# Performance work log

Hardware: AMD Instinct MI355X
Metric: run time of the kernel (lower is better)

Reference implementation:

```python
import jax, jax.numpy as jnp
import numpy as np

N_NODES = 100000
N_EDGES = 1600000
F_IN = 32
F_OUT = 32


def setup_inputs() -> dict:
    key = jax.random.key(0)
    k_x, k_r, k_c, k_v, k_w, k_b = jax.random.split(key, 6)
    x = jax.random.normal(k_x, (N_NODES, F_IN), dtype=jnp.float32)
    edge_rows = jnp.sort(jax.random.randint(k_r, (N_EDGES,), 0, N_NODES, dtype=jnp.int32))
    edge_cols = jax.random.randint(k_c, (N_EDGES,), 0, N_NODES, dtype=jnp.int32)
    edge_vals = jax.random.uniform(k_v, (N_EDGES,), dtype=jnp.float32)
    # nn.Linear params: weight [out, in], bias [out]
    bound = 1.0 / np.sqrt(F_IN)
    W = jax.random.uniform(k_w, (F_OUT, F_IN), minval=-bound, maxval=bound, dtype=jnp.float32)
    b = jax.random.uniform(k_b, (F_OUT,), minval=-bound, maxval=bound, dtype=jnp.float32)
    return {"x": x, "edge_rows": edge_rows, "edge_cols": edge_cols,
            "edge_vals": edge_vals, "W": W, "b": b}


def reference(x, edge_rows, edge_cols, edge_vals, W, b):
    # adj @ x  (COO spmm): gather source features, scale by edge weight,
    # scatter-add into destination rows.
    msgs = x[edge_cols] * edge_vals[:, None]                 # [E, F_in]
    agg = jax.ops.segment_sum(msgs, edge_rows,
                              num_segments=x.shape[0],
                              indices_are_sorted=True)       # [N, F_in]
    # linear + relu: agg @ W.T + b
    return jax.nn.relu(agg @ W.T + b)                        # [N, F_out]
```

## Files before the change

### kernel.cpp

```cpp
#include <hip/hip_runtime.h>

#define F 32

typedef __attribute__((ext_vector_type(8))) unsigned short us8;
typedef __attribute__((ext_vector_type(4))) float f4;

static __device__ __forceinline__ unsigned short f2bf(float f) {
    unsigned int u = __float_as_uint(f);
    u += 0x7FFF + ((u >> 16) & 1);
    return (unsigned short)(u >> 16);
}
static __device__ __forceinline__ float bf2f(unsigned short s) {
    return __uint_as_float(((unsigned int)s) << 16);
}

__global__ __launch_bounds__(256) void prologue_kernel(
    const float* __restrict__ x, const float* __restrict__ W,
    const int* __restrict__ rows,
    unsigned short* __restrict__ y, int* __restrict__ ptr,
    int N, int E, int nxw) {
    int b = blockIdx.x;
    int t = threadIdx.x;
    if (b < nxw) {
        __shared__ float Wt[F * F];
        __shared__ float xs[64 * F];
        #pragma unroll
        for (int k = 0; k < 4; ++k) {
            int i = t + k * 256;
            Wt[(i & 31) * F + (i >> 5)] = W[i];
        }
        int n0 = b * 64;
        const f4* __restrict__ x4 = (const f4*)(x + (size_t)n0 * F);
        f4* __restrict__ xs4 = (f4*)xs;
        int limit4 = (N * F - n0 * F) >> 2;
        #pragma unroll
        for (int k = 0; k < 2; ++k) {
            int i = t + k * 256;
            f4 z = {0.f, 0.f, 0.f, 0.f};
            xs4[i] = (i < limit4) ? x4[i] : z;
        }
        __syncthreads();
        int fo = t & 31;
        int j0 = (t >> 5) * 8;
        #pragma unroll
        for (int j = 0; j < 8; ++j) {
            int nl = j0 + j;
            float acc = 0.0f;
            #pragma unroll
            for (int fi = 0; fi < F; ++fi)
                acc = fmaf(xs[nl * F + fi], Wt[fi * F + fo], acc);
            int n = n0 + nl;
            if (n < N) y[(size_t)n * F + fo] = f2bf(acc);
        }
    } else {
        int e = (b - nxw) * 256 + t;
        if (e > E) return;
        int prev = (e == 0) ? -1 : rows[e - 1];
        int cur  = (e == E) ? N  : rows[e];
        for (int r = prev + 1; r <= cur; ++r) ptr[r] = e;
    }
}

__global__ __launch_bounds__(256) void gnn_kernel(
    const unsigned short* __restrict__ y,
    const int*   __restrict__ cols,
    const float* __restrict__ vals,
    const int*   __restrict__ row_ptr,
    const float* __restrict__ bias,
    float*       __restrict__ out, int N) {
    int t = threadIdx.x;
    int lane = t & 63;
    int g = lane >> 2;
    int l = lane & 3;
    int n = (blockIdx.x * 4 + (t >> 6)) * 16 + g;
    int start = 0, end = 0;
    if (n < N) { start = row_ptr[n]; end = row_ptr[n + 1]; }

    const us8* __restrict__ y8 = (const us8*)y;

    float a0[8], a1[8];
    #pragma unroll
    for (int i = 0; i < 8; ++i) { a0[i] = 0.f; a1[i] = 0.f; }

    for (int e = start; e < end; e += 8) {
        int ec[8];
        #pragma unroll
        for (int k = 0; k < 8; ++k) {
            int ek = e + k;
            ec[k] = (ek < end) ? ek : (end - 1);
        }
        int c[8];
        #pragma unroll
        for (int k = 0; k < 8; ++k) c[k] = cols[ec[k]];
        float v[8];
        #pragma unroll
        for (int k = 0; k < 8; ++k) {
            float vv = vals[ec[k]];
            v[k] = (e + k < end) ? vv : 0.0f;
        }
        us8 r[8];
        #pragma unroll
        for (int k = 0; k < 8; ++k) r[k] = y8[(size_t)c[k] * 4 + l];
        #pragma unroll
        for (int k = 0; k < 8; ++k) {
            float* a = (k & 1) ? a1 : a0;
            #pragma unroll
            for (int i = 0; i < 8; ++i)
                a[i] = fmaf(bf2f(r[k][i]), v[k], a[i]);
        }
    }

    if (n < N) {
        const float* __restrict__ bp = bias + l * 8;
        f4 o0, o1;
        o0.x = fmaxf(a0[0] + a1[0] + bp[0], 0.f);
        o0.y = fmaxf(a0[1] + a1[1] + bp[1], 0.f);
        o0.z = fmaxf(a0[2] + a1[2] + bp[2], 0.f);
        o0.w = fmaxf(a0[3] + a1[3] + bp[3], 0.f);
        o1.x = fmaxf(a0[4] + a1[4] + bp[4], 0.f);
        o1.y = fmaxf(a0[5] + a1[5] + bp[5], 0.f);
        o1.z = fmaxf(a0[6] + a1[6] + bp[6], 0.f);
        o1.w = fmaxf(a0[7] + a1[7] + bp[7], 0.f);
        f4* op = (f4*)(out + (size_t)n * F + l * 8);
        __builtin_nontemporal_store(o0, op);
        __builtin_nontemporal_store(o1, op + 1);
    }
}

__global__ __launch_bounds__(256) void gnn_fp32_kernel(
    const float* __restrict__ x,
    const int*   __restrict__ rows,
    const int*   __restrict__ cols,
    const float* __restrict__ vals,
    const float* __restrict__ W,
    const float* __restrict__ bias,
    float*       __restrict__ out,
    int N, int E) {
    __shared__ float Wt[F * F];
    __shared__ float bS[F];
    int t = threadIdx.x;
    for (int i = t; i < F * F; i += 256)
        Wt[(i & 31) * F + (i >> 5)] = W[i];
    if (t < F) bS[t] = bias[t];
    __syncthreads();
    int lane = t & 63;
    int n = blockIdx.x * 4 + (t >> 6);
    if (n >= N) return;
    int g = lane >> 3, l = lane & 7;
    int target = n + (lane >> 5);
    int lo = 0, hi = E;
    while (lo < hi) { int mid = (lo + hi) >> 1; if (rows[mid] < target) lo = mid + 1; else hi = mid; }
    int start = __shfl(lo, 0), end = __shfl(lo, 32);
    const float4* __restrict__ x4 = (const float4*)x;
    float4 acc0 = {0,0,0,0}, acc1 = {0,0,0,0};
    for (int e0 = start; e0 < end; e0 += 16) {
        int ea = e0 + g, eb = ea + 8;
        if (ea < end) { int c = cols[ea]; float v = vals[ea]; float4 xr = x4[c * 8 + l];
            acc0.x = fmaf(xr.x, v, acc0.x); acc0.y = fmaf(xr.y, v, acc0.y);
            acc0.z = fmaf(xr.z, v, acc0.z); acc0.w = fmaf(xr.w, v, acc0.w); }
        if (eb < end) { int c = cols[eb]; float v = vals[eb]; float4 xr = x4[c * 8 + l];
            acc1.x = fmaf(xr.x, v, acc1.x); acc1.y = fmaf(xr.y, v, acc1.y);
            acc1.z = fmaf(xr.z, v, acc1.z); acc1.w = fmaf(xr.w, v, acc1.w); }
    }
    acc0.x += acc1.x; acc0.y += acc1.y; acc0.z += acc1.z; acc0.w += acc1.w;
    #pragma unroll
    for (int m = 8; m < 64; m <<= 1) {
        acc0.x += __shfl_xor(acc0.x, m); acc0.y += __shfl_xor(acc0.y, m);
        acc0.z += __shfl_xor(acc0.z, m); acc0.w += __shfl_xor(acc0.w, m);
    }
    float comp[4] = {acc0.x, acc0.y, acc0.z, acc0.w};
    int fo = lane & 31;
    float o = bS[fo];
    #pragma unroll
    for (int fi = 0; fi < F; ++fi)
        o = fmaf(__shfl(comp[fi & 3], fi >> 2), Wt[fi * F + fo], o);
    if (lane < F) out[n * F + fo] = fmaxf(o, 0.0f);
}

extern "C" void kernel_launch(void* const* d_in, const int* in_sizes, int n_in,
                              void* d_out, int out_size, void* d_ws, size_t ws_size,
                              hipStream_t stream) {
    const float* x    = (const float*)d_in[0];
    const int*   rows = (const int*)  d_in[1];
    const int*   cols = (const int*)  d_in[2];
    const float* vals = (const float*)d_in[3];
    const float* W    = (const float*)d_in[4];
    const float* bias = (const float*)d_in[5];
    float*       out  = (float*)d_out;

    int N = in_sizes[0] / F;
    int E = in_sizes[1];

    size_t rp_bytes = (size_t)(N + 1) * sizeof(int);
    size_t y_off    = (rp_bytes + 255) & ~(size_t)255;
    size_t need     = y_off + (size_t)N * F * sizeof(unsigned short);

    if (ws_size >= need) {
        int* row_ptr = (int*)d_ws;
        unsigned short* y = (unsigned short*)((char*)d_ws + y_off);
        int nxw  = (N + 63) / 64;
        int ncsr = (E + 1 + 255) / 256;
        prologue_kernel<<<nxw + ncsr, 256, 0, stream>>>(x, W, rows, y, row_ptr, N, E, nxw);
        gnn_kernel<<<(N + 63) / 64, 256, 0, stream>>>(y, cols, vals, row_ptr, bias, out, N);
    } else {
        gnn_fp32_kernel<<<(N + 3) / 4, 256, 0, stream>>>(
            x, rows, cols, vals, W, bias, out, N, E);
    }
}
```

Baseline: 113.5 us.

## Pack col/val pairs in prologue and process two rows per 4-lane group

The prologue now writes interleaved (col, val) int2 pairs into the workspace, so the aggregation kernel does one 8-byte load per edge instead of two separate loads. The aggregation kernel gives each 4-lane group two consecutive rows and walks their combined edge range, routing each edge's weight into one of two accumulators by comparing against the middle row pointer. This halves the number of blocks and balances per-group work across two rows. In exchange the prologue does an extra pass over cols/vals, writing E*8 bytes and growing the workspace. Per-edge FMA work doubles because each edge is multiplied into both accumulators, with zeros for the row it does not belong to.

```diff
diff --git a/kernel.cpp b/kernel.cpp
--- a/kernel.cpp
+++ b/kernel.cpp
@@ -4,6 +4,7 @@
 
 typedef __attribute__((ext_vector_type(8))) unsigned short us8;
 typedef __attribute__((ext_vector_type(4))) float f4;
+typedef __attribute__((ext_vector_type(2))) int i2;
 
 static __device__ __forceinline__ unsigned short f2bf(float f) {
     unsigned int u = __float_as_uint(f);
@@ -17,7 +18,9 @@
 __global__ __launch_bounds__(256) void prologue_kernel(
     const float* __restrict__ x, const float* __restrict__ W,
     const int* __restrict__ rows,
+    const int* __restrict__ cols, const float* __restrict__ vals,
     unsigned short* __restrict__ y, int* __restrict__ ptr,
+    i2* __restrict__ packed,
     int N, int E, int nxw) {
     int b = blockIdx.x;
     int t = threadIdx.x;
@@ -54,27 +57,38 @@
         }
     } else {
         int e = (b - nxw) * 256 + t;
-        if (e > E) return;
-        int prev = (e == 0) ? -1 : rows[e - 1];
-        int cur  = (e == E) ? N  : rows[e];
-        for (int r = prev + 1; r <= cur; ++r) ptr[r] = e;
+        if (e <= E) {
+            int prev = (e == 0) ? -1 : rows[e - 1];
+            int cur  = (e == E) ? N  : rows[e];
+            for (int r = prev + 1; r <= cur; ++r) ptr[r] = e;
+        }
+        if (e < E) {
+            i2 p;
+            p.x = cols[e];
+            p.y = __float_as_int(vals[e]);
+            packed[e] = p;
+        }
     }
 }
 
 __global__ __launch_bounds__(256) void gnn_kernel(
     const unsigned short* __restrict__ y,
-    const int*   __restrict__ cols,
-    const float* __restrict__ vals,
-    const int*   __restrict__ row_ptr,
+    const i2*  __restrict__ packed,
+    const int* __restrict__ row_ptr,
     const float* __restrict__ bias,
     float*       __restrict__ out, int N) {
     int t = threadIdx.x;
     int lane = t & 63;
     int g = lane >> 2;
     int l = lane & 3;
-    int n = (blockIdx.x * 4 + (t >> 6)) * 16 + g;
-    int start = 0, end = 0;
-    if (n < N) { start = row_ptr[n]; end = row_ptr[n + 1]; }
+    int base = (blockIdx.x * 4 + (t >> 6)) * 32;
+    int na = base + 2 * g;
+    int ia = na     < N ? na     : N;
+    int ib = na + 1 < N ? na + 1 : N;
+    int ic = na + 2 < N ? na + 2 : N;
+    int s0 = row_ptr[ia];
+    int s1 = row_ptr[ib];
+    int s2 = row_ptr[ic];
 
     const us8* __restrict__ y8 = (const us8*)y;
 
@@ -82,46 +96,66 @@
     #pragma unroll
     for (int i = 0; i < 8; ++i) { a0[i] = 0.f; a1[i] = 0.f; }
 
-    for (int e = start; e < end; e += 8) {
-        int ec[8];
+    for (int e = s0; e < s2; e += 8) {
+        int ee[8];
         #pragma unroll
         for (int k = 0; k < 8; ++k) {
             int ek = e + k;
-            ec[k] = (ek < end) ? ek : (end - 1);
-        }
-        int c[8];
-        #pragma unroll
-        for (int k = 0; k < 8; ++k) c[k] = cols[ec[k]];
-        float v[8];
+            ee[k] = (ek < s2) ? ek : (s2 - 1);
+        }
+        i2 p[8];
+        #pragma unroll
+        for (int k = 0; k < 8; ++k)
+            p[k] = __builtin_nontemporal_load(&packed[ee[k]]);
+        float va[8], vb[8];
         #pragma unroll
         for (int k = 0; k < 8; ++k) {
-            float vv = vals[ec[k]];
-            v[k] = (e + k < end) ? vv : 0.0f;
+            float v = __int_as_float(p[k].y);
+            int ek = e + k;
+            va[k] = (ek < s1) ? v : 0.f;
+            vb[k] = (ek >= s1 && ek < s2) ? v : 0.f;
         }
         us8 r[8];
         #pragma unroll
-        for (int k = 0; k < 8; ++k) r[k] = y8[(size_t)c[k] * 4 + l];
+        for (int k = 0; k < 8; ++k)
+            r[k] = y8[(p[k].x << 2) + l];
         #pragma unroll
         for (int k = 0; k < 8; ++k) {
-            float* a = (k & 1) ? a1 : a0;
             #pragma unroll
-            for (int i = 0; i < 8; ++i)
-                a[i] = fmaf(bf2f(r[k][i]), v[k], a[i]);
-        }
-    }
-
-    if (n < N) {
-        const float* __restrict__ bp = bias + l * 8;
+            for (int i = 0; i < 8; ++i) {
+                float xf = bf2f(r[k][i]);
+                a0[i] = fmaf(xf, va[k], a0[i]);
+                a1[i] = fmaf(xf, vb[k], a1[i]);
+            }
+        }
+    }
+
+    const float* __restrict__ bp = bias + l * 8;
+    if (na < N) {
         f4 o0, o1;
-        o0.x = fmaxf(a0[0] + a1[0] + bp[0], 0.f);
-        o0.y = fmaxf(a0[1] + a1[1] + bp[1], 0.f);
-        o0.z = fmaxf(a0[2] + a1[2] + bp[2], 0.f);
-        o0.w = fmaxf(a0[3] + a1[3] + bp[3], 0.f);
-        o1.x = fmaxf(a0[4] + a1[4] + bp[4], 0.f);
-        o1.y = fmaxf(a0[5] + a1[5] + bp[5], 0.f);
-        o1.z = fmaxf(a0[6] + a1[6] + bp[6], 0.f);
-        o1.w = fmaxf(a0[7] + a1[7] + bp[7], 0.f);
-        f4* op = (f4*)(out + (size_t)n * F + l * 8);
+        o0.x = fmaxf(a0[0] + bp[0], 0.f);
+        o0.y = fmaxf(a0[1] + bp[1], 0.f);
+        o0.z = fmaxf(a0[2] + bp[2], 0.f);
+        o0.w = fmaxf(a0[3] + bp[3], 0.f);
+        o1.x = fmaxf(a0[4] + bp[4], 0.f);
+        o1.y = fmaxf(a0[5] + bp[5], 0.f);
+        o1.z = fmaxf(a0[6] + bp[6], 0.f);
+        o1.w = fmaxf(a0[7] + bp[7], 0.f);
+        f4* op = (f4*)(out + (size_t)na * F + l * 8);
+        __builtin_nontemporal_store(o0, op);
+        __builtin_nontemporal_store(o1, op + 1);
+    }
+    if (na + 1 < N) {
+        f4 o0, o1;
+        o0.x = fmaxf(a1[0] + bp[0], 0.f);
+        o0.y = fmaxf(a1[1] + bp[1], 0.f);
+        o0.z = fmaxf(a1[2] + bp[2], 0.f);
+        o0.w = fmaxf(a1[3] + bp[3], 0.f);
+        o1.x = fmaxf(a1[4] + bp[4], 0.f);
+        o1.y = fmaxf(a1[5] + bp[5], 0.f);
+        o1.z = fmaxf(a1[6] + bp[6], 0.f);
+        o1.w = fmaxf(a1[7] + bp[7], 0.f);
+        f4* op = (f4*)(out + (size_t)(na + 1) * F + l * 8);
         __builtin_nontemporal_store(o0, op);
         __builtin_nontemporal_store(o1, op + 1);
     }
@@ -192,16 +226,20 @@
     int E = in_sizes[1];
 
     size_t rp_bytes = (size_t)(N + 1) * sizeof(int);
-    size_t y_off    = (rp_bytes + 255) & ~(size_t)255;
+    size_t pk_off   = (rp_bytes + 255) & ~(size_t)255;
+    size_t y_off    = (pk_off + (size_t)E * 8 + 255) & ~(size_t)255;
     size_t need     = y_off + (size_t)N * F * sizeof(unsigned short);
 
     if (ws_size >= need) {
         int* row_ptr = (int*)d_ws;
+        i2*  packed  = (i2*)((char*)d_ws + pk_off);
         unsigned short* y = (unsigned short*)((char*)d_ws + y_off);
         int nxw  = (N + 63) / 64;
         int ncsr = (E + 1 + 255) / 256;
-        prologue_kernel<<<nxw + ncsr, 256, 0, stream>>>(x, W, rows, y, row_ptr, N, E, nxw);
-        gnn_kernel<<<(N + 63) / 64, 256, 0, stream>>>(y, cols, vals, row_ptr, bias, out, N);
+        prologue_kernel<<<nxw + ncsr, 256, 0, stream>>>(
+            x, W, rows, cols, vals, y, row_ptr, packed, N, E, nxw);
+        gnn_kernel<<<(N + 127) / 128, 256, 0, stream>>>(
+            y, packed, row_ptr, bias, out, N);
     } else {
         gnn_fp32_kernel<<<(N + 3) / 4, 256, 0, stream>>>(
             x, rows, cols, vals, W, bias, out, N, E);
```

Measured after the change: 129.2 us. 13.8% more time.
